# Kernel optimization log

Measured on AMD Instinct MI355X. Metric: run time of the kernel, lower is better.

Reference implementation:

```python
import jax, jax.numpy as jnp
import numpy as np

H = 16       # num_attention_heads
DH = 64      # attention_head_size
D = H * DH   # hidden_size = 1024
SCALE = DH ** -0.5


def setup_inputs() -> dict:
    key = jax.random.key(0)
    ks = jax.random.split(key, 9)
    s = 0.02
    return {
        "hidden_states": jax.random.normal(ks[0], (2, 2048, D), jnp.float32),
        "Wq": jax.random.normal(ks[1], (D, D), jnp.float32) * s,
        "bq": jax.random.normal(ks[2], (D,), jnp.float32) * s,
        "Wk": jax.random.normal(ks[3], (D, D), jnp.float32) * s,
        "bk": jax.random.normal(ks[4], (D,), jnp.float32) * s,
        "Wv": jax.random.normal(ks[5], (D, D), jnp.float32) * s,
        "bv": jax.random.normal(ks[6], (D,), jnp.float32) * s,
        "Wo": jax.random.normal(ks[7], (D, D), jnp.float32) * s,
        "bo": jax.random.normal(ks[8], (D,), jnp.float32) * s,
    }


def reference(hidden_states, Wq, bq, Wk, bk, Wv, bv, Wo, bo):
    B, S, _ = hidden_states.shape
    # project and split into heads: [B, H, S, DH]
    def heads(x):
        return x.reshape(B, S, H, DH).transpose(0, 2, 1, 3)
    q = heads(hidden_states @ Wq + bq)
    k = heads(hidden_states @ Wk + bk)
    v = heads(hidden_states @ Wv + bv)
    # eager attention: full [B,H,S,S] scores, softmax in fp32
    scores = jnp.einsum("bhqd,bhkd->bhqk", q, k) * SCALE
    probs = jax.nn.softmax(scores.astype(jnp.float32), axis=-1).astype(q.dtype)
    ctx = jnp.einsum("bhqk,bhkd->bqhd", probs, v).reshape(B, S, D)
    # output projection (dropout inactive at eval)
    return ctx @ Wo + bo
```

## Files before the change

### kernel.cpp

```cpp
#include <hip/hip_runtime.h>

typedef __bf16 bf16;
typedef __bf16 bf16x8 __attribute__((ext_vector_type(8)));
typedef __bf16 bf16x4 __attribute__((ext_vector_type(4)));
typedef float  f32x4  __attribute__((ext_vector_type(4)));
typedef unsigned u32x2 __attribute__((ext_vector_type(2)));
typedef unsigned u32x4 __attribute__((ext_vector_type(4)));

#define DEV __device__ __forceinline__

DEV int detect_f32(const void* x) {
  const unsigned short* u = (const unsigned short*)x;
  int cnt = 0;
#pragma unroll 8
  for (int i = 0; i < 512; i += 2) {
    int e = (u[i] >> 7) & 0xFF;
    cnt += (e >= 118 && e <= 134) ? 1 : 0;
  }
  return cnt < 128;
}

DEV void gl2lds16(const bf16* g, bf16* l) {
  __builtin_amdgcn_global_load_lds(
      (const __attribute__((address_space(1))) void*)g,
      (__attribute__((address_space(3))) void*)l, 16, 0, 0);
}

DEV unsigned pack_bf16(float a, float b) {
  unsigned ua = __float_as_uint(a) + 0x8000u;
  unsigned ub = __float_as_uint(b) + 0x8000u;
  return __builtin_amdgcn_perm(ub, ua, 0x07060302u);
}

__global__ __launch_bounds__(256) void prep(
    const void* __restrict__ X, const void* __restrict__ bq,
    const void* __restrict__ bk, const void* __restrict__ bv,
    const void* __restrict__ bo, const void* __restrict__ Wq,
    const void* __restrict__ Wk, const void* __restrict__ Wv,
    const void* __restrict__ Wo, bf16* __restrict__ Xb,
    bf16* __restrict__ bqkv, bf16* __restrict__ bob,
    bf16* __restrict__ Wtqkv, bf16* __restrict__ Wto) {
  __shared__ __align__(16) bf16 T[64 * 80];
  int f32 = detect_f32(X);
  int blk = blockIdx.x, tid = threadIdx.x;
  if (blk < 2048) {
    long base = (long)blk * 2048 + tid * 8;
    bf16x8 o;
    if (f32) {
      const float* s = (const float*)X + base;
#pragma unroll
      for (int i = 0; i < 8; ++i) o[i] = (bf16)s[i];
    } else {
      o = *(const bf16x8*)((const bf16*)X + base);
    }
    *(bf16x8*)&Xb[base] = o;
  } else if (blk < 2052) {
    const void* src = (blk == 2048) ? bq : (blk == 2049) ? bk : (blk == 2050) ? bv : bo;
    bf16* dst = (blk == 2051) ? bob : bqkv + (blk - 2048) * 1024;
    int base = tid * 4;
    if (f32) {
      const float* s = (const float*)src;
#pragma unroll
      for (int i = 0; i < 4; ++i) dst[base + i] = (bf16)s[base + i];
    } else {
      const bf16* s = (const bf16*)src;
#pragma unroll
      for (int i = 0; i < 4; ++i) dst[base + i] = s[base + i];
    }
  } else {
    int id = blk - 2052;
    int z = id >> 8, r = id & 255;
    int k0 = (r & 15) * 64, n0 = (r >> 4) * 64;
    const void* src = (z == 0) ? Wq : (z == 1) ? Wk : (z == 2) ? Wv : Wo;
    bf16* dst = (z < 3) ? (Wtqkv + (long)z * 1048576) : Wto;
#pragma unroll
    for (int c = 0; c < 2; ++c) {
      int lin = tid + c * 256;
      int row = lin >> 3, col8 = (lin & 7) * 8;
      long gidx = (long)(k0 + row) * 1024 + n0 + col8;
      bf16x8 v;
      if (f32) {
        const float* s = (const float*)src + gidx;
#pragma unroll
        for (int i = 0; i < 8; ++i) v[i] = (bf16)s[i];
      } else {
        v = *(const bf16x8*)((const bf16*)src + gidx);
      }
      *(bf16x8*)&T[row * 80 + col8] = v;
    }
    __syncthreads();
#pragma unroll
    for (int c = 0; c < 2; ++c) {
      int lin = tid + c * 256;
      int row = lin >> 3, col8 = (lin & 7) * 8;
      bf16x8 v;
#pragma unroll
      for (int i = 0; i < 8; ++i) v[i] = T[(col8 + i) * 80 + row];
      *(bf16x8*)&dst[(long)(n0 + row) * 1024 + k0 + col8] = v;
    }
  }
}

template <int TM, int MODE>
__global__ __launch_bounds__(256, 3) void gemm_bt(
    const bf16* __restrict__ A, const bf16* __restrict__ Bt, int M, int N,
    int K, void* __restrict__ Cout, const bf16* __restrict__ bias,
    const void* __restrict__ detect_src, bf16* __restrict__ Qo,
    bf16* __restrict__ Ko, bf16* __restrict__ Vo) {
  constexpr int MT = TM / 32;
  __shared__ __align__(16) bf16 GS[TM * 64 + 128 * 64];
  bf16* As = GS;
  bf16* Bs = GS + TM * 64;
  int tid = threadIdx.x, lane = tid & 63, wave = tid >> 6;
  int quad = lane >> 4, l16 = lane & 15;
  int m0 = blockIdx.x * TM, n0 = blockIdx.y * 128;
  int wm = (wave >> 1) * (TM / 2), wn = (wave & 1) * 64;
  f32x4 zero = {0.f, 0.f, 0.f, 0.f};
  f32x4 acc[MT][4];
#pragma unroll
  for (int i = 0; i < MT; ++i)
#pragma unroll
    for (int j = 0; j < 4; ++j) acc[i][j] = zero;

  for (int k0 = 0; k0 < K; k0 += 64) {
#pragma unroll
    for (int i = 0; i < MT; ++i) {
      int u = (i * 4 + wave) * 64 + lane;
      int r = u >> 3, g = (u & 7) ^ (r & 7);
      gl2lds16(A + (long)(m0 + r) * K + k0 + g * 8, As + (i * 4 + wave) * 512);
    }
#pragma unroll
    for (int i = 0; i < 4; ++i) {
      int u = (i * 4 + wave) * 64 + lane;
      int r = u >> 3, g = (u & 7) ^ (r & 7);
      gl2lds16(Bt + (long)(n0 + r) * K + k0 + g * 8, Bs + (i * 4 + wave) * 512);
    }
    __syncthreads();
#pragma unroll
    for (int kc = 0; kc < 2; ++kc) {
      bf16x8 bv_[4];
#pragma unroll
      for (int nt = 0; nt < 4; ++nt) {
        int row = wn + nt * 16 + l16;
        bv_[nt] = *(const bf16x8*)&Bs[row * 64 + (((kc * 4 + quad) ^ (l16 & 7))) * 8];
      }
#pragma unroll
      for (int mt = 0; mt < MT; ++mt) {
        int row = wm + mt * 16 + l16;
        bf16x8 af = *(const bf16x8*)&As[row * 64 + (((kc * 4 + quad) ^ (l16 & 7))) * 8];
#pragma unroll
        for (int nt = 0; nt < 4; ++nt)
          acc[mt][nt] = __builtin_amdgcn_mfma_f32_16x16x32_bf16(bv_[nt], af,
                                                                acc[mt][nt], 0, 0, 0);
      }
    }
    __syncthreads();
  }

  if (MODE == 0) {
    int f32o = detect_f32(detect_src);
#pragma unroll
    for (int nt = 0; nt < 4; ++nt) {
      int n = n0 + wn + nt * 16 + quad * 4;
      bf16x4 bb = *(const bf16x4*)&bias[n];
#pragma unroll
      for (int mt = 0; mt < MT; ++mt) {
        int m = m0 + wm + mt * 16 + l16;
        if (f32o) {
          f32x4 v;
#pragma unroll
          for (int r = 0; r < 4; ++r) v[r] = acc[mt][nt][r] + (float)bb[r];
          *(f32x4*)((float*)Cout + (long)m * N + n) = v;
        } else {
          bf16x4 v;
#pragma unroll
          for (int r = 0; r < 4; ++r) v[r] = (bf16)(acc[mt][nt][r] + (float)bb[r]);
          *(bf16x4*)((bf16*)Cout + (long)m * N + n) = v;
        }
      }
    }
  } else {
    int t = n0 >> 10;
    if (t < 2) {
      float qsc = (t == 0) ? 0.1803368801f : 1.0f;
      bf16* op = (t == 0) ? Qo : Ko;
#pragma unroll
      for (int nt = 0; nt < 4; ++nt) {
        int n = n0 + wn + nt * 16 + quad * 4;
        bf16x4 bb = *(const bf16x4*)&bias[n];
        int nl = n & 1023, h = nl >> 6, dh = nl & 63;
#pragma unroll
        for (int mt = 0; mt < MT; ++mt) {
          int m = m0 + wm + mt * 16 + l16;
          int b = m >> 11, s = m & 2047;
          bf16x4 v;
#pragma unroll
          for (int r = 0; r < 4; ++r)
            v[r] = (bf16)((acc[mt][nt][r] + (float)bb[r]) * qsc);
          *(bf16x4*)&op[((long)(b * 16 + h) * 2048 + s) * 64 + dh] = v;
        }
      }
    } else {
      bf16* T = GS;
#pragma unroll
      for (int nt = 0; nt < 4; ++nt) {
        int n = wn + nt * 16 + quad * 4;
        bf16x4 bb = *(const bf16x4*)&bias[n0 + n];
#pragma unroll
        for (int mt = 0; mt < MT; ++mt) {
          int m = wm + mt * 16 + l16;
#pragma unroll
          for (int r = 0; r < 4; ++r)
            T[(n + r) * 128 + m] = (bf16)(acc[mt][nt][r] + (float)bb[r]);
        }
      }
      __syncthreads();
      int b = m0 >> 11, s0 = m0 & 2047;
      int h0 = (n0 & 1023) >> 6;
#pragma unroll
      for (int c = 0; c < 8; ++c) {
        int u = c * 256 + tid;
        int row = u >> 4, col = (u & 15) * 8;
        bf16x8 v = *(const bf16x8*)&T[row * 128 + col];
        long base =
            ((long)(b * 16 + h0 + (row >> 6)) * 64 + (row & 63)) * 2048 + s0;
        *(bf16x8*)&Vo[base + col] = v;
      }
    }
  }
}

__global__ __launch_bounds__(512, 4) void attn(const bf16* __restrict__ Qg,
                                               const bf16* __restrict__ Kg,
                                               const bf16* __restrict__ Vtg,
                                               bf16* __restrict__ ctx) {
  __shared__ __align__(16) bf16 SMEM[32768];
  bf16* Ksh = SMEM;
  bf16* Vsh = SMEM + 16384;
  float* MG = (float*)SMEM;

  int tid = threadIdx.x, lane = tid & 63, w = tid >> 6;
  int grp = w >> 2, wq = w & 3;
  int quad = lane >> 4, l16 = lane & 15;
  int bh = blockIdx.y, q0 = blockIdx.x * 128;
  const bf16* Qh = Qg + (long)bh * 131072;
  const bf16* Kh = Kg + (long)bh * 131072;
  const bf16* Vh = Vtg + (long)bh * 131072;
  int qbase = q0 + wq * 32;

  bf16x8 qf[2][2];
#pragma unroll
  for (int nt = 0; nt < 2; ++nt)
#pragma unroll
    for (int kc = 0; kc < 2; ++kc)
      qf[nt][kc] = *(const bf16x8*)&Qh[(long)(qbase + nt * 16 + l16) * 64 +
                                       kc * 32 + quad * 8];

  int e0 = l16 * 64 + (quad ^ (l16 & 7)) * 8;
  int e1 = l16 * 64 + ((4 + quad) ^ (l16 & 7)) * 8;

  f32x4 zero = {0.f, 0.f, 0.f, 0.f};
  f32x4 O[2][4];
  f32x4 ls4[2] = {zero, zero};
#pragma unroll
  for (int i = 0; i < 2; ++i)
#pragma unroll
    for (int j = 0; j < 4; ++j) O[i][j] = zero;

#define STAGE2(ta)                                                            \
  {                                                                           \
    _Pragma("unroll") for (int j = 0; j < 4; ++j) {                           \
      int unit = j * 512 + tid;                                               \
      int tile = (ta) + (unit >> 10);                                         \
      if (tile < 32) {                                                        \
        int u = unit & 1023, buf = tile & 3;                                  \
        if (u < 512) {                                                        \
          int m = u >> 3, g = (u & 7) ^ (m & 7);                              \
          int kvp = (m & 32) + ((m & 12) << 1) + ((m & 16) >> 2) + (m & 3);   \
          gl2lds16(Kh + (long)(tile * 64 + kvp) * 64 + g * 8,                 \
                   Ksh + buf * 4096 + u * 8);                                 \
        } else {                                                              \
          int v = u - 512;                                                    \
          int m = v >> 3, g = (v & 7) ^ (m & 7);                              \
          gl2lds16(Vh + (long)m * 2048 + tile * 64 + g * 8,                   \
                   Vsh + buf * 4096 + v * 8);                                 \
        }                                                                     \
      }                                                                       \
    }                                                                         \
  }

  auto compute = [&](const bf16* Kb, const bf16* Vb) {
    u32x2 pk[4][2];
#pragma unroll
    for (int mt = 0; mt < 4; ++mt) {
      bf16x8 kf0 = *(const bf16x8*)&Kb[e0 + mt * 1024];
      bf16x8 kf1 = *(const bf16x8*)&Kb[e1 + mt * 1024];
#pragma unroll
      for (int nt = 0; nt < 2; ++nt) {
        f32x4 s_ = zero;
        s_ = __builtin_amdgcn_mfma_f32_16x16x32_bf16(kf0, qf[nt][0], s_, 0, 0, 0);
        s_ = __builtin_amdgcn_mfma_f32_16x16x32_bf16(kf1, qf[nt][1], s_, 0, 0, 0);
        f32x4 p;
        p[0] = __builtin_amdgcn_exp2f(s_[0]);
        p[1] = __builtin_amdgcn_exp2f(s_[1]);
        p[2] = __builtin_amdgcn_exp2f(s_[2]);
        p[3] = __builtin_amdgcn_exp2f(s_[3]);
        ls4[nt] += p;
        pk[mt][nt][0] = pack_bf16(p[0], p[1]);
        pk[mt][nt][1] = pack_bf16(p[2], p[3]);
      }
    }
#pragma unroll
    for (int c = 0; c < 2; ++c) {
      bf16x8 pb[2];
#pragma unroll
      for (int nt = 0; nt < 2; ++nt) {
        u32x4 tt;
        tt[0] = pk[2 * c][nt][0];
        tt[1] = pk[2 * c][nt][1];
        tt[2] = pk[2 * c + 1][nt][0];
        tt[3] = pk[2 * c + 1][nt][1];
        pb[nt] = __builtin_bit_cast(bf16x8, tt);
      }
      int ec = c ? e1 : e0;
#pragma unroll
      for (int dt = 0; dt < 4; ++dt) {
        bf16x8 vf = *(const bf16x8*)&Vb[ec + dt * 1024];
#pragma unroll
        for (int nt = 0; nt < 2; ++nt)
          O[nt][dt] = __builtin_amdgcn_mfma_f32_16x16x32_bf16(vf, pb[nt],
                                                              O[nt][dt], 0, 0, 0);
      }
    }
  };

  STAGE2(0);
  for (int it = 0; it < 16; ++it) {
    __syncthreads();
    STAGE2(2 * it + 2);
    int t = 2 * it + grp;
    compute(Ksh + (t & 3) * 4096, Vsh + (t & 3) * 4096);
  }

  float lsum[2];
#pragma unroll
  for (int nt = 0; nt < 2; ++nt)
    lsum[nt] = (ls4[nt][0] + ls4[nt][1]) + (ls4[nt][2] + ls4[nt][3]);

  __syncthreads();
  float* Mp = MG + wq * 2176;
  if (grp == 1) {
#pragma unroll
    for (int nt = 0; nt < 2; ++nt) {
#pragma unroll
      for (int dt = 0; dt < 4; ++dt)
        *(f32x4*)&Mp[((nt * 4 + dt) * 64 + lane) * 4] = O[nt][dt];
      Mp[2048 + nt * 64 + lane] = lsum[nt];
    }
  }
  __syncthreads();
  if (grp == 0) {
#pragma unroll
    for (int nt = 0; nt < 2; ++nt) {
#pragma unroll
      for (int dt = 0; dt < 4; ++dt) {
        f32x4 o2 = *(const f32x4*)&Mp[((nt * 4 + dt) * 64 + lane) * 4];
#pragma unroll
        for (int r = 0; r < 4; ++r) O[nt][dt][r] += o2[r];
      }
      lsum[nt] += Mp[2048 + nt * 64 + lane];
    }
    float rv[2];
#pragma unroll
    for (int nt = 0; nt < 2; ++nt) {
      float s = lsum[nt];
      s += __shfl_xor(s, 16, 64);
      s += __shfl_xor(s, 32, 64);
      rv[nt] = __builtin_amdgcn_rcpf(s);
    }
    int b = bh >> 4, h = bh & 15;
#pragma unroll
    for (int nt = 0; nt < 2; ++nt) {
      int s = qbase + nt * 16 + l16;
#pragma unroll
      for (int dt = 0; dt < 4; ++dt) {
        bf16x4 v;
#pragma unroll
        for (int r = 0; r < 4; ++r) v[r] = (bf16)(O[nt][dt][r] * rv[nt]);
        *(bf16x4*)&ctx[((long)(b * 2048 + s)) * 1024 + h * 64 + dt * 16 +
                       quad * 4] = v;
      }
    }
  }
}

extern "C" void kernel_launch(void* const* d_in, const int* in_sizes, int n_in,
                              void* d_out, int out_size, void* d_ws,
                              size_t ws_size, hipStream_t stream) {
  const void* X  = d_in[0];
  const void* Wq = d_in[1]; const void* bq = d_in[2];
  const void* Wk = d_in[3]; const void* bk = d_in[4];
  const void* Wv = d_in[5]; const void* bv = d_in[6];
  const void* Wo = d_in[7]; const void* bo = d_in[8];

  char* ws = (char*)d_ws;
  bf16* Xb    = (bf16*)(ws);
  bf16* Wtqkv = (bf16*)(ws + 8388608);
  bf16* Wto   = (bf16*)(ws + 14680064);
  bf16* bqkv  = (bf16*)(ws + 16777216);
  bf16* bob   = (bf16*)(ws + 16783360);
  bf16* Qw    = (bf16*)(ws + 16785408);
  bf16* Kw    = (bf16*)(ws + 25174016);
  bf16* Cx    = (bf16*)(ws + 33562624);
  bf16* Vt    = (bf16*)(ws + 41951232);

  prep<<<dim3(3076), 256, 0, stream>>>(X, bq, bk, bv, bo, Wq, Wk, Wv, Wo, Xb,
                                       bqkv, bob, Wtqkv, Wto);
  gemm_bt<128, 1><<<dim3(32, 24), 256, 0, stream>>>(
      Xb, Wtqkv, 4096, 3072, 1024, nullptr, bqkv, nullptr, Qw, Kw, Vt);
  attn<<<dim3(16, 32), 512, 0, stream>>>(Qw, Kw, Vt, Cx);
  gemm_bt<64, 0><<<dim3(64, 8), 256, 0, stream>>>(
      Cx, Wto, 4096, 1024, 1024, d_out, bob, X, nullptr, nullptr, nullptr);
}
```

Baseline: 218.6 us.

## Compute softmax row sums via MFMA, swizzle block order, add setprio, ballot detection

The softmax denominator is now accumulated with an extra MFMA against a ones vector, using the bf16-rounded probabilities, instead of per-lane VALU adds plus cross-lane shuffles. Blocks are remapped with a swizzle so neighbouring workgroups spread across heads, s_setprio is raised around the MFMA sections, and input-dtype detection uses a wave ballot rather than a serial loop. bf16 packing now uses the compiler's conversion (round-to-nearest-even) instead of the add-and-permute trick. Together these aim to trim VALU work and improve scheduling and cache locality, at the cost of extra matrix ops per tile.

```diff
diff --git a/kernel.cpp b/kernel.cpp
--- a/kernel.cpp
+++ b/kernel.cpp
@@ -3,6 +3,7 @@
 typedef __bf16 bf16;
 typedef __bf16 bf16x8 __attribute__((ext_vector_type(8)));
 typedef __bf16 bf16x4 __attribute__((ext_vector_type(4)));
+typedef __bf16 bf16x2 __attribute__((ext_vector_type(2)));
 typedef float  f32x4  __attribute__((ext_vector_type(4)));
 typedef unsigned u32x2 __attribute__((ext_vector_type(2)));
 typedef unsigned u32x4 __attribute__((ext_vector_type(4)));
@@ -11,13 +12,10 @@
 
 DEV int detect_f32(const void* x) {
   const unsigned short* u = (const unsigned short*)x;
-  int cnt = 0;
-#pragma unroll 8
-  for (int i = 0; i < 512; i += 2) {
-    int e = (u[i] >> 7) & 0xFF;
-    cnt += (e >= 118 && e <= 134) ? 1 : 0;
-  }
-  return cnt < 128;
+  int lane = threadIdx.x & 63;
+  int e = (u[lane * 8] >> 7) & 0xFF;
+  unsigned long long b = __ballot(e >= 118 && e <= 134);
+  return __popcll(b) < 32;
 }
 
 DEV void gl2lds16(const bf16* g, bf16* l) {
@@ -27,9 +25,10 @@
 }
 
 DEV unsigned pack_bf16(float a, float b) {
-  unsigned ua = __float_as_uint(a) + 0x8000u;
-  unsigned ub = __float_as_uint(b) + 0x8000u;
-  return __builtin_amdgcn_perm(ub, ua, 0x07060302u);
+  bf16x2 t;
+  t[0] = (bf16)a;
+  t[1] = (bf16)b;
+  return __builtin_bit_cast(unsigned, t);
 }
 
 __global__ __launch_bounds__(256) void prep(
@@ -242,7 +241,9 @@
   int tid = threadIdx.x, lane = tid & 63, w = tid >> 6;
   int grp = w >> 2, wq = w & 3;
   int quad = lane >> 4, l16 = lane & 15;
-  int bh = blockIdx.y, q0 = blockIdx.x * 128;
+  int lin = blockIdx.x | (blockIdx.y << 4);
+  int swz = ((lin & 7) << 6) | (lin >> 3);
+  int bh = swz >> 4, q0 = (swz & 15) << 7;
   const bf16* Qh = Qg + (long)bh * 131072;
   const bf16* Kh = Kg + (long)bh * 131072;
   const bf16* Vh = Vtg + (long)bh * 131072;
@@ -259,9 +260,13 @@
   int e0 = l16 * 64 + (quad ^ (l16 & 7)) * 8;
   int e1 = l16 * 64 + ((4 + quad) ^ (l16 & 7)) * 8;
 
+  bf16x8 onesv;
+#pragma unroll
+  for (int i = 0; i < 8; ++i) onesv[i] = (bf16)1.0f;
+
   f32x4 zero = {0.f, 0.f, 0.f, 0.f};
   f32x4 O[2][4];
-  f32x4 ls4[2] = {zero, zero};
+  f32x4 Ol[2] = {zero, zero};
 #pragma unroll
   for (int i = 0; i < 2; ++i)
 #pragma unroll
@@ -298,14 +303,15 @@
 #pragma unroll
       for (int nt = 0; nt < 2; ++nt) {
         f32x4 s_ = zero;
+        __builtin_amdgcn_s_setprio(1);
         s_ = __builtin_amdgcn_mfma_f32_16x16x32_bf16(kf0, qf[nt][0], s_, 0, 0, 0);
         s_ = __builtin_amdgcn_mfma_f32_16x16x32_bf16(kf1, qf[nt][1], s_, 0, 0, 0);
+        __builtin_amdgcn_s_setprio(0);
         f32x4 p;
         p[0] = __builtin_amdgcn_exp2f(s_[0]);
         p[1] = __builtin_amdgcn_exp2f(s_[1]);
         p[2] = __builtin_amdgcn_exp2f(s_[2]);
         p[3] = __builtin_amdgcn_exp2f(s_[3]);
-        ls4[nt] += p;
         pk[mt][nt][0] = pack_bf16(p[0], p[1]);
         pk[mt][nt][1] = pack_bf16(p[2], p[3]);
       }
@@ -323,6 +329,7 @@
         pb[nt] = __builtin_bit_cast(bf16x8, tt);
       }
       int ec = c ? e1 : e0;
+      __builtin_amdgcn_s_setprio(1);
 #pragma unroll
       for (int dt = 0; dt < 4; ++dt) {
         bf16x8 vf = *(const bf16x8*)&Vb[ec + dt * 1024];
@@ -331,6 +338,11 @@
           O[nt][dt] = __builtin_amdgcn_mfma_f32_16x16x32_bf16(vf, pb[nt],
                                                               O[nt][dt], 0, 0, 0);
       }
+#pragma unroll
+      for (int nt = 0; nt < 2; ++nt)
+        Ol[nt] = __builtin_amdgcn_mfma_f32_16x16x32_bf16(onesv, pb[nt],
+                                                         Ol[nt], 0, 0, 0);
+      __builtin_amdgcn_s_setprio(0);
     }
   };
 
@@ -342,10 +354,7 @@
     compute(Ksh + (t & 3) * 4096, Vsh + (t & 3) * 4096);
   }
 
-  float lsum[2];
-#pragma unroll
-  for (int nt = 0; nt < 2; ++nt)
-    lsum[nt] = (ls4[nt][0] + ls4[nt][1]) + (ls4[nt][2] + ls4[nt][3]);
+  float lsum[2] = {Ol[0][0], Ol[1][0]};
 
   __syncthreads();
   float* Mp = MG + wq * 2176;
@@ -372,12 +381,7 @@
     }
     float rv[2];
 #pragma unroll
-    for (int nt = 0; nt < 2; ++nt) {
-      float s = lsum[nt];
-      s += __shfl_xor(s, 16, 64);
-      s += __shfl_xor(s, 32, 64);
-      rv[nt] = __builtin_amdgcn_rcpf(s);
-    }
+    for (int nt = 0; nt < 2; ++nt) rv[nt] = __builtin_amdgcn_rcpf(lsum[nt]);
     int b = bh >> 4, h = bh & 15;
 #pragma unroll
     for (int nt = 0; nt < 2; ++nt) {
```

New measurement: 184.2 us. -15.7%, faster.
